# Kernel optimization log

Measured on AMD Instinct MI355X. Metric: run time of the kernel, lower is better.

Reference implementation:

```python
import jax, jax.numpy as jnp
import numpy as np

TEMPERATURE = 0.5   # cfg.LOSS.TEMPERATURE
REG = 0.5           # Sinkhorn entropic regularization
NUM_ITER = 100      # numItermax in forward call
STOP_THR = 1e-9

BS, NUM_CLASSES, DIM = 16384, 1000, 512


def _l2norm(x):
    return x / jnp.linalg.norm(x, axis=-1, keepdims=True)


def setup_inputs() -> dict:
    key = jax.random.key(0)
    k1, k2, k3 = jax.random.split(key, 3)
    features = _l2norm(jax.random.normal(k1, (BS, DIM), jnp.float32))
    text_features = _l2norm(jax.random.normal(k2, (NUM_CLASSES, DIM), jnp.float32))
    ratios = jax.random.uniform(k3, (NUM_CLASSES,), jnp.float32)
    ratios = ratios / ratios.sum()  # class prior, sums to 1
    return {"features": features, "text_features": text_features, "ratios": ratios}


def sinkhorn_knopp(a, b, M, reg):
    """Faithful Sinkhorn-Knopp: u/v scaling loop with NaN/Inf bail-out and
    every-10-iters convergence check, unrolled as a masked lax.scan."""
    dim_a, dim_b = a.shape[0], b.shape[0]
    K = jnp.exp(M / -reg)                 # [dim_a, dim_b]
    Kp = (1.0 / a)[:, None] * K           # [dim_a, dim_b]
    u0 = jnp.ones((dim_a,), M.dtype) / dim_a
    v0 = jnp.ones((dim_b,), M.dtype) / dim_b

    def step(carry, ii):
        u, v, done = carry
        KtU = K.T @ u                     # [dim_b]
        v_new = b / KtU
        u_new = 1.0 / (Kp @ v_new)        # [dim_a]
        bad = (jnp.any(KtU == 0)
               | jnp.any(~jnp.isfinite(u_new))
               | jnp.any(~jnp.isfinite(v_new)))
        # err check (original does it when ii % 10 == 0)
        tmp2 = (u_new @ K) * v_new        # einsum('i,ij,j->j', u, K, v)
        err = jnp.linalg.norm(tmp2 - b)
        converged = ((ii % 10) == 0) & (err < STOP_THR)
        keep_prev = done | bad            # revert to uprev/vprev on bad, freeze after done
        u2 = jnp.where(keep_prev, u, u_new)
        v2 = jnp.where(keep_prev, v, v_new)
        return (u2, v2, done | bad | converged), None

    (u, v, _), _ = jax.lax.scan(step, (u0, v0, jnp.array(False)), jnp.arange(NUM_ITER))
    return u[:, None] * K * v[None, :]


def reference(features, text_features, ratios):
    sim_matrix = (features @ text_features.T) / TEMPERATURE   # [bs, C]
    cost_matrix = 1.0 - sim_matrix
    bs = features.shape[0]
    a = jnp.ones((bs,), features.dtype)       # row marginal (uniform over batch)
    b = ratios * bs                            # column marginal (class ratios)
    plan = sinkhorn_knopp(a, b, sim_matrix / cost_matrix, REG)  # [bs, C]
    return plan
```

## Files before the change

kernel.cpp:

```cpp
#include <hip/hip_runtime.h>
#include <hip/hip_bf16.h>

typedef float   f32x4_t  __attribute__((ext_vector_type(4)));
typedef float   f32x2_t  __attribute__((ext_vector_type(2)));
typedef __bf16  bf16x8_t __attribute__((ext_vector_type(8)));
typedef int     i32x4_t  __attribute__((ext_vector_type(4)));

#define N_ROWS   16384
#define N_COLS   1000
#define N_COLS_P 1024
#define N_DIM    512
#define N_ITER   100
#define PBLK     256
#define PTHR     512
#define NRED     64

__device__ __forceinline__ float ldf_sc1(const float* p) {
    return __hip_atomic_load(p, __ATOMIC_RELAXED, __HIP_MEMORY_SCOPE_AGENT);
}
__device__ __forceinline__ void stf_sc1(float* p, float v) {
    __hip_atomic_store(p, v, __ATOMIC_RELAXED, __HIP_MEMORY_SCOPE_AGENT);
}
__device__ __forceinline__ int ldi_sc1(const int* p) {
    return __hip_atomic_load(p, __ATOMIC_RELAXED, __HIP_MEMORY_SCOPE_AGENT);
}
__device__ __forceinline__ void sti_sc1(int* p, int v) {
    __hip_atomic_store(p, v, __ATOMIC_RELAXED, __HIP_MEMORY_SCOPE_AGENT);
}
__device__ __forceinline__ void st2_sc1(float* p, float a, float b) {
    const unsigned long long u =
        ((unsigned long long)__builtin_bit_cast(unsigned, b) << 32) |
        __builtin_bit_cast(unsigned, a);
    __hip_atomic_store((unsigned long long*)p, u, __ATOMIC_RELAXED,
                       __HIP_MEMORY_SCOPE_AGENT);
}
__device__ __forceinline__ void drain_vmem() {
    asm volatile("s_waitcnt vmcnt(0)" ::: "memory");
}

__device__ __forceinline__ unsigned short f2bf(float f) {
    unsigned int u = __builtin_bit_cast(unsigned int, f);
    u += 0x7FFFu + ((u >> 16) & 1u);
    return (unsigned short)(u >> 16);
}

template <int MODE>
__launch_bounds__(256)
__global__ void k_gemm(const float* __restrict__ F, const float* __restrict__ T,
                       void* __restrict__ Kout, float* __restrict__ cpart,
                       const float* __restrict__ v_com, const float* __restrict__ u_both,
                       const int* __restrict__ flags)
{
    __shared__ unsigned short lA[128 * 72];
    __shared__ unsigned short lB[128 * 72];
    __shared__ float cs_lds[4 * 64];

    const int bm = blockIdx.x;
    const int bn = blockIdx.y;
    const int m0 = bm << 7;
    const int n0 = bn << 7;
    const int t  = threadIdx.x;
    const int lane = t & 63;
    const int wid  = t >> 6;
    const int wr = wid >> 1;
    const int wc = wid & 1;

    f32x4_t acc[4][4];
#pragma unroll
    for (int a = 0; a < 4; ++a)
#pragma unroll
        for (int b = 0; b < 4; ++b)
            acc[a][b] = (f32x4_t){0.f, 0.f, 0.f, 0.f};

    const int srow = t >> 4;
    const int scol = (t & 15) << 2;

    for (int kt = 0; kt < N_DIM; kt += 64) {
#pragma unroll
        for (int r = 0; r < 8; ++r) {
            const int rr = srow + (r << 4);
            const float4 av = *(const float4*)(F + (size_t)(m0 + rr) * N_DIM + kt + scol);
            ushort4 a4; a4.x = f2bf(av.x); a4.y = f2bf(av.y); a4.z = f2bf(av.z); a4.w = f2bf(av.w);
            *(ushort4*)(&lA[rr * 72 + scol]) = a4;
            const int gn = n0 + rr;
            float4 bv = make_float4(0.f, 0.f, 0.f, 0.f);
            if (gn < N_COLS) bv = *(const float4*)(T + (size_t)gn * N_DIM + kt + scol);
            ushort4 b4; b4.x = f2bf(bv.x); b4.y = f2bf(bv.y); b4.z = f2bf(bv.z); b4.w = f2bf(bv.w);
            *(ushort4*)(&lB[rr * 72 + scol]) = b4;
        }
        __syncthreads();
#pragma unroll
        for (int ks = 0; ks < 2; ++ks) {
            bf16x8_t afr[4], bfr[4];
#pragma unroll
            for (int mf = 0; mf < 4; ++mf) {
                const int r = (wr << 6) + (mf << 4) + (lane & 15);
                const int off = r * 72 + (ks << 5) + ((lane >> 4) << 3);
                afr[mf] = __builtin_bit_cast(bf16x8_t, *(const i32x4_t*)(&lA[off]));
            }
#pragma unroll
            for (int nf = 0; nf < 4; ++nf) {
                const int r = (wc << 6) + (nf << 4) + (lane & 15);
                const int off = r * 72 + (ks << 5) + ((lane >> 4) << 3);
                bfr[nf] = __builtin_bit_cast(bf16x8_t, *(const i32x4_t*)(&lB[off]));
            }
#pragma unroll
            for (int mf = 0; mf < 4; ++mf)
#pragma unroll
                for (int nf = 0; nf < 4; ++nf)
                    acc[mf][nf] = __builtin_amdgcn_mfma_f32_16x16x32_bf16(
                        afr[mf], bfr[nf], acc[mf][nf], 0, 0, 0);
        }
        __syncthreads();
    }

    int usel = 2;
    if (MODE == 1) usel = flags[1];
    float csum[4] = {0.f, 0.f, 0.f, 0.f};
#pragma unroll
    for (int mf = 0; mf < 4; ++mf) {
#pragma unroll
        for (int nf = 0; nf < 4; ++nf) {
#pragma unroll
            for (int j = 0; j < 4; ++j) {
                const float d = acc[mf][nf][j];
                const float s = 2.f * d;
                const float M = s / (1.f - s);
                const float kv = __expf(-2.f * M);
                const int grow = m0 + (wr << 6) + (mf << 4) + ((lane >> 4) << 2) + j;
                const int gcol = n0 + (wc << 6) + (nf << 4) + (lane & 15);
                if (MODE == 0) {
                    ((unsigned short*)Kout)[(size_t)grow * N_COLS_P + gcol] =
                        (gcol < N_COLS) ? f2bf(kv) : (unsigned short)0;
                    csum[nf] += kv;
                } else {
                    if (gcol < N_COLS) {
                        const float u = (usel == 2) ? (1.f / 16384.f)
                                                    : u_both[(size_t)usel * N_ROWS + grow];
                        ((float*)Kout)[(size_t)grow * N_COLS + gcol] = u * kv * v_com[gcol];
                    }
                }
            }
        }
    }
    if (MODE == 0) {
#pragma unroll
        for (int nf = 0; nf < 4; ++nf) {
            csum[nf] += __shfl_xor(csum[nf], 16);
            csum[nf] += __shfl_xor(csum[nf], 32);
        }
        if (lane < 16) {
#pragma unroll
            for (int nf = 0; nf < 4; ++nf)
                cs_lds[wid * 64 + (nf << 4) + lane] = csum[nf];
        }
        __syncthreads();
        if (t < 128) {
            const int cw = t >> 6;
            const int c6 = t & 63;
            cpart[(size_t)bm * N_COLS_P + n0 + t] =
                cs_lds[cw * 64 + c6] + cs_lds[(cw + 2) * 64 + c6];
        }
    }
}

__launch_bounds__(128)
__global__ void k_init(const float* __restrict__ cpart, float* __restrict__ ktu0,
                       float* __restrict__ vcom, int* __restrict__ flags,
                       int* __restrict__ pready, int* __restrict__ rready,
                       int* __restrict__ flags2)
{
    const int j = blockIdx.x * 128 + threadIdx.x;
    if (j < N_COLS) {
        float s = 0.f;
        for (int p = 0; p < 128; ++p) s += cpart[(size_t)p * N_COLS_P + j];
        ktu0[j] = s * (1.f / 16384.f);
        vcom[j] = 1.f / 1000.f;
    } else {
        ktu0[j] = 1.f;
        vcom[j] = 0.f;
    }
    if (j < PBLK) pready[j] = 0;
    if (j < NRED) rready[j] = 0;
    if (j < 128)  flags2[j] = 0;
    if (j < 4)    flags[j] = (j == 1) ? 2 : 0;
}

__launch_bounds__(PTHR, 2)
__global__ void k_persist(const unsigned short* __restrict__ Kb,
                          const float* __restrict__ ratios,
                          float* __restrict__ ktu,
                          float* __restrict__ utmp,
                          float* __restrict__ vcom,
                          float* __restrict__ partials,
                          int* __restrict__ flags,
                          int* __restrict__ pready,
                          int* __restrict__ rready,
                          int* __restrict__ flags2)
{
    __shared__ float vbuf[2][N_COLS_P];
    __shared__ float wp[8][N_COLS_P];
    __shared__ float redw[8][16];
    __shared__ float rbc;
    __shared__ int ibc;
    const int t = threadIdx.x, lane = t & 63, wid = t >> 6, b = blockIdx.x;
    const int row0 = (b << 6) + (wid << 3);
    const bool isred = (b < NRED);

    unsigned kp[8][8];
#pragma unroll
    for (int r = 0; r < 8; ++r) {
        const unsigned* rp = (const unsigned*)(Kb + (size_t)(row0 + r) * N_COLS_P);
#pragma unroll
        for (int q = 0; q < 8; ++q) kp[r][q] = rp[(q << 6) + lane];
    }
    const float bj0 = (t < N_COLS) ? ratios[t] * 16384.f : 0.f;
    const float bj1 = (t + PTHR < N_COLS) ? ratios[t + PTHR] * 16384.f : 0.f;

    int usel = 2;

    for (int ii = 0; ii <= N_ITER; ++ii) {
        const int p = ii & 1;
        float kc0, kc1;

        if (ii > 0) {
            if (wid == 0) {
                for (;;) {
                    const int ok = (ldi_sc1(&rready[lane]) >= ii);
                    if (__all(ok)) break;
                    __builtin_amdgcn_s_sleep(1);
                }
            }
            __syncthreads();
            if (t == 0) ibc = ldi_sc1(&flags2[ii - 1]);
            __syncthreads();
            if (ibc) break;
            usel = (ii - 1) & 1;
            kc0 = ldf_sc1(&ktu[(p << 10) + t]);
            kc1 = ldf_sc1(&ktu[(p << 10) + t + PTHR]);
            if (((ii - 1) % 10) == 0) {
                const float vo0 = vbuf[usel][t], vo1 = vbuf[usel][t + PTHR];
                const float d0 = (t < N_COLS) ? kc0 * vo0 - bj0 : 0.f;
                const float d1 = (t + PTHR < N_COLS) ? kc1 * vo1 - bj1 : 0.f;
                float e = d0 * d0 + d1 * d1;
#pragma unroll
                for (int sh = 1; sh <= 32; sh <<= 1) e += __shfl_xor(e, sh);
                if (lane == 0) redw[wid][0] = e;
                __syncthreads();
                if (t == 0) {
                    float s = 0.f;
#pragma unroll
                    for (int w = 0; w < 8; ++w) s += redw[w][0];
                    rbc = s;
                }
                __syncthreads();
                if (rbc < 1e-18f) break;
            }
            if (ii == N_ITER) break;
        } else {
            kc0 = ldf_sc1(&ktu[t]);
            kc1 = ldf_sc1(&ktu[t + PTHR]);
        }

        const float v0 = bj0 / kc0;
        const float v1 = bj1 / kc1;
        const int badv = (kc0 == 0.f) | (kc1 == 0.f) | (!isfinite(v0)) | (!isfinite(v1));
        vbuf[p][t] = v0;
        vbuf[p][t + PTHR] = v1;
        if (__syncthreads_or(badv)) break;

        float vr[16];
#pragma unroll
        for (int q = 0; q < 8; ++q) {
            const f32x2_t vv = *(const f32x2_t*)&vbuf[p][(q << 7) + (lane << 1)];
            vr[2*q] = vv[0]; vr[2*q+1] = vv[1];
        }
        float dots[8];
#pragma unroll
        for (int r = 0; r < 8; ++r) {
            float p0 = 0.f, p1 = 0.f, p2 = 0.f, p3 = 0.f;
#pragma unroll
            for (int q = 0; q < 8; ++q) {
                const unsigned u = kp[r][q];
                const float lo = __builtin_bit_cast(float, u << 16);
                const float hi = __builtin_bit_cast(float, u & 0xFFFF0000u);
                if (q & 1) { p2 = fmaf(lo, vr[2*q], p2); p3 = fmaf(hi, vr[2*q+1], p3); }
                else       { p0 = fmaf(lo, vr[2*q], p0); p1 = fmaf(hi, vr[2*q+1], p1); }
            }
            dots[r] = (p0 + p1) + (p2 + p3);
        }
#pragma unroll
        for (int s = 1; s <= 32; s <<= 1) {
#pragma unroll
            for (int r = 0; r < 8; ++r) dots[r] += __shfl_xor(dots[r], s);
        }
        float u8[8];
        int ubad = 0;
#pragma unroll
        for (int r = 0; r < 8; ++r) { u8[r] = 1.f / dots[r]; ubad |= !isfinite(u8[r]); }
        if (lane == 0) {
            float* uo = utmp + ((size_t)p << 14) + row0;
#pragma unroll
            for (int r = 0; r < 8; ++r) uo[r] = u8[r];
        }
        if (__any(ubad) && lane == 0)
            __hip_atomic_fetch_or(&flags2[ii], 1, __ATOMIC_RELAXED,
                                  __HIP_MEMORY_SCOPE_AGENT);

        float creg[16];
#pragma unroll
        for (int e = 0; e < 16; ++e) creg[e] = 0.f;
#pragma unroll
        for (int r = 0; r < 8; ++r) {
#pragma unroll
            for (int q = 0; q < 8; ++q) {
                const unsigned u = kp[r][q];
                const float lo = __builtin_bit_cast(float, u << 16);
                const float hi = __builtin_bit_cast(float, u & 0xFFFF0000u);
                creg[2*q]   = fmaf(lo, u8[r], creg[2*q]);
                creg[2*q+1] = fmaf(hi, u8[r], creg[2*q+1]);
            }
        }
#pragma unroll
        for (int q = 0; q < 8; ++q)
            *(f32x2_t*)&wp[wid][(q << 7) + (lane << 1)] = (f32x2_t){creg[2*q], creg[2*q+1]};
        __syncthreads();
        {
            const int j2 = t << 1;
            f32x2_t s2 = *(const f32x2_t*)&wp[0][j2];
#pragma unroll
            for (int w = 1; w < 8; ++w) {
                const f32x2_t x = *(const f32x2_t*)&wp[w][j2];
                s2[0] += x[0]; s2[1] += x[1];
            }
            st2_sc1(&partials[((size_t)b << 10) + j2], s2[0], s2[1]);
        }
        drain_vmem();
        __syncthreads();
        if (t == 0) sti_sc1(&pready[b], ii + 1);

        if (isred) {
            if (wid == 0) {
                for (;;) {
                    int ok = 1;
#pragma unroll
                    for (int h = 0; h < 4; ++h)
                        ok &= (ldi_sc1(&pready[(h << 6) + lane]) >= ii + 1);
                    if (__all(ok)) break;
                }
            }
            __syncthreads();
            const int col = (b << 4) + (t & 15);
            const int pr0 = t >> 4;
            float s = 0.f;
#pragma unroll
            for (int k = 0; k < 8; ++k)
                s += ldf_sc1(&partials[((size_t)(pr0 + (k << 5)) << 10) + col]);
            s += __shfl_xor(s, 16);
            s += __shfl_xor(s, 32);
            if (lane < 16) redw[wid][lane] = s;
            __syncthreads();
            if (t < 16) {
                float s2 = 0.f;
#pragma unroll
                for (int w = 0; w < 8; ++w) s2 += redw[w][t];
                const int c = (b << 4) + t;
                stf_sc1(&ktu[(((ii + 1) & 1) << 10) + c], (c < N_COLS) ? s2 : 1.f);
            }
            drain_vmem();
            __syncthreads();
            if (t == 0) sti_sc1(&rready[b], ii + 1);
        }
    }

    if (b == 0) {
        float vf0, vf1;
        if (usel == 2) { vf0 = 1.f / 1000.f; vf1 = 1.f / 1000.f; }
        else           { vf0 = vbuf[usel][t]; vf1 = vbuf[usel][t + PTHR]; }
        if (t < N_COLS) vcom[t] = vf0;
        if (t + PTHR < N_COLS) vcom[t + PTHR] = vf1;
        if (t == 0) flags[1] = usel;
    }
}

extern "C" void kernel_launch(void* const* d_in, const int* in_sizes, int n_in,
                              void* d_out, int out_size, void* d_ws, size_t ws_size,
                              hipStream_t stream)
{
    const float* F      = (const float*)d_in[0];
    const float* T      = (const float*)d_in[1];
    const float* ratios = (const float*)d_in[2];
    float* out = (float*)d_out;
    unsigned short* Kb = (unsigned short*)d_out;

    float* ws        = (float*)d_ws;
    float* partials  = ws;
    float* ktu       = partials + (size_t)PBLK * N_COLS_P;
    float* utmp      = ktu + 2 * N_COLS_P;
    float* vcom      = utmp + 2 * N_ROWS;
    int*   flags     = (int*)(vcom + N_COLS_P);
    int*   pready    = flags + 4;
    int*   rready    = pready + PBLK;
    int*   flags2    = rready + NRED;
    const size_t need_bytes = ((size_t)PBLK * N_COLS_P + 2 * N_COLS_P + 2 * N_ROWS +
                               N_COLS_P) * sizeof(float) +
                              (4 + PBLK + NRED + 128) * sizeof(int);
    if (ws_size < need_bytes) return;

    k_gemm<0><<<dim3(128, 8), 256, 0, stream>>>(F, T, Kb, partials, nullptr, nullptr, flags);
    k_init<<<8, 128, 0, stream>>>(partials, ktu, vcom, flags, pready, rready, flags2);
    k_persist<<<PBLK, PTHR, 0, stream>>>(Kb, ratios, ktu, utmp, vcom, partials,
                                         flags, pready, rready, flags2);
    k_gemm<1><<<dim3(128, 8), 256, 0, stream>>>(F, T, out, nullptr, vcom, utmp, flags);
}
```

Before: 2.245 ms.

## Replace per-block ready flags with padded flags and atomic counter barrier

After: 2.133 ms. -5.0%, faster.

```diff
diff --git a/kernel.cpp b/kernel.cpp
--- a/kernel.cpp
+++ b/kernel.cpp
@@ -167,7 +167,7 @@
 __launch_bounds__(128)
 __global__ void k_init(const float* __restrict__ cpart, float* __restrict__ ktu0,
                        float* __restrict__ vcom, int* __restrict__ flags,
-                       int* __restrict__ pready, int* __restrict__ rready,
+                       int* __restrict__ pst, int* __restrict__ rcnt,
                        int* __restrict__ flags2)
 {
     const int j = blockIdx.x * 128 + threadIdx.x;
@@ -180,10 +180,9 @@
         ktu0[j] = 1.f;
         vcom[j] = 0.f;
     }
-    if (j < PBLK) pready[j] = 0;
-    if (j < NRED) rready[j] = 0;
-    if (j < 128)  flags2[j] = 0;
-    if (j < 4)    flags[j] = (j == 1) ? 2 : 0;
+    for (int z = j; z < PBLK * 16; z += 1024) pst[z] = 0;
+    if (j < 128) { rcnt[j] = 0; flags2[j] = 0; }
+    if (j < 4)   flags[j] = (j == 1) ? 2 : 0;
 }
 
 __launch_bounds__(PTHR, 2)
@@ -194,8 +193,8 @@
                           float* __restrict__ vcom,
                           float* __restrict__ partials,
                           int* __restrict__ flags,
-                          int* __restrict__ pready,
-                          int* __restrict__ rready,
+                          int* __restrict__ pst,
+                          int* __restrict__ rcnt,
                           int* __restrict__ flags2)
 {
     __shared__ float vbuf[2][N_COLS_P];
@@ -224,15 +223,10 @@
         float kc0, kc1;
 
         if (ii > 0) {
-            if (wid == 0) {
-                for (;;) {
-                    const int ok = (ldi_sc1(&rready[lane]) >= ii);
-                    if (__all(ok)) break;
-                    __builtin_amdgcn_s_sleep(1);
-                }
-            }
-            __syncthreads();
-            if (t == 0) ibc = ldi_sc1(&flags2[ii - 1]);
+            if (t == 0) {
+                while (ldi_sc1(&rcnt[ii - 1]) < NRED) __builtin_amdgcn_s_sleep(1);
+                ibc = ldi_sc1(&flags2[ii - 1]);
+            }
             __syncthreads();
             if (ibc) break;
             usel = (ii - 1) & 1;
@@ -337,25 +331,24 @@
         }
         drain_vmem();
         __syncthreads();
-        if (t == 0) sti_sc1(&pready[b], ii + 1);
+        if (t == 0) sti_sc1(&pst[b << 4], ii + 1);
 
         if (isred) {
-            if (wid == 0) {
+            {
+                const int prod = (wid << 5) + (lane & 31);
+                const int pidx = prod << 4;
                 for (;;) {
-                    int ok = 1;
-#pragma unroll
-                    for (int h = 0; h < 4; ++h)
-                        ok &= (ldi_sc1(&pready[(h << 6) + lane]) >= ii + 1);
+                    const int ok = (lane < 32) ? (ldi_sc1(&pst[pidx]) >= ii + 1) : 1;
                     if (__all(ok)) break;
+                    __builtin_amdgcn_s_sleep(2);
                 }
             }
-            __syncthreads();
-            const int col = (b << 4) + (t & 15);
-            const int pr0 = t >> 4;
+            const int col = (b << 4) + (lane & 15);
+            const int r0 = (wid << 5) + (lane >> 4);
             float s = 0.f;
 #pragma unroll
             for (int k = 0; k < 8; ++k)
-                s += ldf_sc1(&partials[((size_t)(pr0 + (k << 5)) << 10) + col]);
+                s += ldf_sc1(&partials[((size_t)(r0 + (k << 2)) << 10) + col]);
             s += __shfl_xor(s, 16);
             s += __shfl_xor(s, 32);
             if (lane < 16) redw[wid][lane] = s;
@@ -369,7 +362,9 @@
             }
             drain_vmem();
             __syncthreads();
-            if (t == 0) sti_sc1(&rready[b], ii + 1);
+            if (t == 0)
+                __hip_atomic_fetch_add(&rcnt[ii], 1, __ATOMIC_RELAXED,
+                                       __HIP_MEMORY_SCOPE_AGENT);
         }
     }
 
@@ -399,17 +394,17 @@
     float* utmp      = ktu + 2 * N_COLS_P;
     float* vcom      = utmp + 2 * N_ROWS;
     int*   flags     = (int*)(vcom + N_COLS_P);
-    int*   pready    = flags + 4;
-    int*   rready    = pready + PBLK;
-    int*   flags2    = rready + NRED;
+    int*   pst       = flags + 4;
+    int*   rcnt      = pst + PBLK * 16;
+    int*   flags2    = rcnt + 128;
     const size_t need_bytes = ((size_t)PBLK * N_COLS_P + 2 * N_COLS_P + 2 * N_ROWS +
                                N_COLS_P) * sizeof(float) +
-                              (4 + PBLK + NRED + 128) * sizeof(int);
+                              (4 + PBLK * 16 + 128 + 128) * sizeof(int);
     if (ws_size < need_bytes) return;
 
     k_gemm<0><<<dim3(128, 8), 256, 0, stream>>>(F, T, Kb, partials, nullptr, nullptr, flags);
-    k_init<<<8, 128, 0, stream>>>(partials, ktu, vcom, flags, pready, rready, flags2);
+    k_init<<<8, 128, 0, stream>>>(partials, ktu, vcom, flags, pst, rcnt, flags2);
     k_persist<<<PBLK, PTHR, 0, stream>>>(Kb, ratios, ktu, utmp, vcom, partials,
-                                         flags, pready, rready, flags2);
+                                         flags, pst, rcnt, flags2);
     k_gemm<1><<<dim3(128, 8), 256, 0, stream>>>(F, T, out, nullptr, vcom, utmp, flags);
 }
```
